# Kernel tuning notes

Hardware: AMD Instinct MI355X
Metric: run time of the kernel (lower is better)

## Reference

```python
import jax, jax.numpy as jnp
import numpy as np
from jax import lax

NUM_COARSE = 64
GROUP_SIZE = 32
GRID_SIZE = 6
GRID_PTS = GRID_SIZE * GRID_SIZE  # 36


def setup_inputs() -> dict:
    key = jax.random.key(0)
    ki = iter(jax.random.split(key, 64))

    def rn(shape, scale=0.02):
        return jax.random.normal(next(ki), shape, jnp.float32) * scale

    B, N = 8, 8192
    return {
        "corrupted_pts": jax.random.normal(next(ki), (B, N, 3), jnp.float32),
        "pts": jax.random.normal(next(ki), (B, N, 3), jnp.float32),
        "enc_w1": rn((3, 128)), "enc_b1": jnp.zeros((128,), jnp.float32),
        "enc_w2": rn((128, 256)), "enc_b2": jnp.zeros((256,), jnp.float32),
        "enc_w3": rn((256, 1024)), "enc_b3": jnp.zeros((1024,), jnp.float32),
        "pe_w1": rn((3, 128)), "pe_b1": jnp.zeros((128,), jnp.float32),
        "pe_w2": rn((128, 1024)), "pe_b2": jnp.zeros((1024,), jnp.float32),
        "cp_w1": rn((1024, 1024)), "cp_b1": jnp.zeros((1024,), jnp.float32),
        "cp_w2": rn((1024, 1024)), "cp_b2": jnp.zeros((1024,), jnp.float32),
        "cp_w3": rn((1024, NUM_COARSE * 3)), "cp_b3": jnp.zeros((NUM_COARSE * 3,), jnp.float32),
        "f1_w1": rn((1024 + 2, 512)), "f1_b1": jnp.zeros((512,), jnp.float32),
        "f1_w2": rn((512, 512)), "f1_b2": jnp.zeros((512,), jnp.float32),
        "f1_w3": rn((512, 3)), "f1_b3": jnp.zeros((3,), jnp.float32),
        "f2_w1": rn((1024 + 3, 512)), "f2_b1": jnp.zeros((512,), jnp.float32),
        "f2_w2": rn((512, 512)), "f2_b2": jnp.zeros((512,), jnp.float32),
        "f2_w3": rn((512, 3)), "f2_b3": jnp.zeros((3,), jnp.float32),
    }


def _fps(xyz, n_samples):
    """Farthest point sampling, start at index 0. xyz: (N,3) -> (n_samples,3)."""
    d0 = jnp.sum((xyz - xyz[0]) ** 2, axis=-1)

    def step(dists, _):
        nxt = jnp.argmax(dists)
        d = jnp.sum((xyz - xyz[nxt]) ** 2, axis=-1)
        return jnp.minimum(dists, d), nxt

    _, idxs = lax.scan(step, d0, None, length=n_samples - 1)
    idxs = jnp.concatenate([jnp.zeros((1,), idxs.dtype), idxs])
    return xyz[idxs]


def _chamfer_l2(x, y):
    """Symmetric Chamfer-L2 over batched point sets x:(B,Nx,3), y:(B,Ny,3)."""
    d = jnp.sum((x[:, :, None, :] - y[:, None, :, :]) ** 2, axis=-1)  # (B,Nx,Ny)
    return jnp.mean(jnp.min(d, axis=2)) + jnp.mean(jnp.min(d, axis=1))


def _build_grid():
    # itertools.product(x, y): x varies slowest -> 'ij' meshgrid ordering
    lin = jnp.linspace(-0.3, 0.3, GRID_SIZE)
    xx, yy = jnp.meshgrid(lin, lin, indexing="ij")
    return jnp.stack([xx.ravel(), yy.ravel()], axis=-1)  # (36,2)


def reference(corrupted_pts, pts,
              enc_w1, enc_b1, enc_w2, enc_b2, enc_w3, enc_b3,
              pe_w1, pe_b1, pe_w2, pe_b2,
              cp_w1, cp_b1, cp_w2, cp_b2, cp_w3, cp_b3,
              f1_w1, f1_b1, f1_w2, f1_b2, f1_w3, f1_b3,
              f2_w1, f2_b1, f2_w2, f2_b2, f2_w3, f2_b3):
    corrupted_pts = corrupted_pts[:, :, :3]
    pts = pts[:, :, :3]
    B, N, _ = pts.shape

    # --- Group divider: FPS centers + KNN neighborhoods (normalized) ---
    centers = jax.vmap(lambda p: _fps(p, NUM_COARSE))(pts)            # (B,G,3)
    d2 = jnp.sum((centers[:, :, None, :] - pts[:, None, :, :]) ** 2, axis=-1)  # (B,G,N)
    _, idx = lax.top_k(-d2, GROUP_SIZE)                               # (B,G,K)
    neigh = jnp.take_along_axis(pts[:, None, :, :], idx[..., None], axis=2)    # (B,G,K,3)
    neigh = neigh - centers[:, :, None, :]

    # --- positional embedding of centers ---
    pos = jax.nn.gelu(centers @ pe_w1 + pe_b1, approximate=False) @ pe_w2 + pe_b2  # (B,G,1024)

    # --- global encoder (PointNet-style stand-in for PointNetv2_encoder) ---
    h = jax.nn.relu(corrupted_pts @ enc_w1 + enc_b1)
    h = jax.nn.relu(h @ enc_w2 + enc_b2)
    h = h @ enc_w3 + enc_b3
    feat = jnp.max(h, axis=1)                                          # (B,1024)

    # --- coarse prediction ---
    c = jax.nn.relu(feat @ cp_w1 + cp_b1)
    c = jax.nn.relu(c @ cp_w2 + cp_b2)
    coarse = (c @ cp_w3 + cp_b3).reshape(B, NUM_COARSE, 3)

    # --- folding decoder (1x1 convs == per-point linears) ---
    BG = B * NUM_COARSE
    fe = (feat[:, None, :] + pos).reshape(BG, 1024)
    fe = jnp.broadcast_to(fe[:, None, :], (BG, GRID_PTS, 1024))
    grid = jnp.broadcast_to(_build_grid()[None], (BG, GRID_PTS, 2))
    cat1 = jnp.concatenate([fe, grid], axis=-1)                        # (BG,36,1026)
    h1 = jax.nn.relu(cat1 @ f1_w1 + f1_b1)
    h1 = jax.nn.relu(h1 @ f1_w2 + f1_b2)
    fold1 = h1 @ f1_w3 + f1_b3                                         # (BG,36,3)
    cat2 = jnp.concatenate([fe, fold1], axis=-1)                       # (BG,36,1027)
    h2 = jax.nn.relu(cat2 @ f2_w1 + f2_b1)
    h2 = jax.nn.relu(h2 @ f2_w2 + f2_b2)
    fold2 = h2 @ f2_w3 + f2_b3                                         # (BG,36,3)

    loss_coarse = _chamfer_l2(coarse, centers)
    loss_fine = _chamfer_l2(fold2, neigh.reshape(BG, GROUP_SIZE, 3))
    return (loss_fine, loss_coarse)
```

## Files before the change

### kernel.cpp

```cpp
#include <hip/hip_runtime.h>
#include <float.h>
#include <math.h>

typedef unsigned short u16;
typedef short bshort8 __attribute__((ext_vector_type(8)));
typedef float vf4 __attribute__((ext_vector_type(4)));

struct Ptrs { const float* p[30]; };

__device__ __align__(16) unsigned int g_featkey[8192];
__device__ __align__(16) float g_fold1[18432 * 3];
__device__ __align__(16) float g_fold2[18432 * 3];
__device__ __align__(16) float g_accum[8];
__device__ __align__(16) float g_centers[512 * 3];
__device__ __align__(16) float g_neigh[512 * 32 * 3];
__device__ __align__(16) float g_c1[8192];
__device__ __align__(16) float g_c2[8192];
__device__ __align__(16) float g_coarse[8 * 192];
__device__ __align__(16) u16 g_p1[512 * 128];
__device__ __align__(16) u16 g_fe[512 * 1024];
__device__ __align__(16) u16 g_fea[512 * 512];
__device__ __align__(16) u16 g_feb[512 * 512];
__device__ __align__(16) float g_gw[36 * 512];
__device__ __align__(16) u16 g_w2T[256 * 128];
__device__ __align__(16) u16 g_w3T[1024 * 256];
__device__ __align__(16) u16 g_pew2T[1024 * 128];
__device__ __align__(16) u16 g_f1w1aT[512 * 1024];
__device__ __align__(16) u16 g_f1w2T[512 * 512];
__device__ __align__(16) u16 g_f2w1aT[512 * 1024];
__device__ __align__(16) u16 g_f2w2T[512 * 512];

__device__ __forceinline__ u16 f2b(float f) {
    unsigned int u = __float_as_uint(f);
    unsigned int r = (u + 0x7fffu + ((u >> 16) & 1u)) >> 16;
    return (u16)r;
}
__device__ __forceinline__ float b2f(u16 u) {
    return __uint_as_float(((unsigned int)u) << 16);
}
__device__ __forceinline__ float dec(unsigned int k) {
    unsigned int u = (k & 0x80000000u) ? (k & 0x7fffffffu) : ~k;
    return __uint_as_float(u);
}

__global__ __launch_bounds__(256) void zero_kernel(Ptrs ptrs, u16* out) {
    int i = blockIdx.x * 256 + threadIdx.x;
    if (i < 8192) {
        g_featkey[i] = 0u;
        g_c1[i] = 0.f;
        g_c2[i] = 0.f;
    }
    if (i < 1536) g_coarse[i] = 0.f;
    if (i < 18432 * 3) { g_fold1[i] = 0.f; g_fold2[i] = 0.f; }
    if (i < 8) g_accum[i] = 0.f;
}

__global__ __launch_bounds__(256) void convert_kernel(Ptrs ptrs, u16* out) {
    int plane = blockIdx.y;
    if (plane == 7) {
        int id = blockIdx.x * 256 + threadIdx.x;
        if (id >= 36 * 512) return;
        const float* f1w1 = ptrs.p[18];
        const float* f1b1 = ptrs.p[19];
        int q = id >> 9, n = id & 511;
        int qi = q / 6, qj = q - qi * 6;
        float gx = (qi == 5) ? 0.3f : (-0.3f + qi * 0.12f);
        float gy = (qj == 5) ? 0.3f : (-0.3f + qj * 0.12f);
        g_gw[id] = gx * f1w1[(size_t)1024 * 512 + n] + gy * f1w1[(size_t)1025 * 512 + n] + f1b1[n];
        return;
    }
    static const int kSrc[7] = {4, 6, 10, 18, 20, 24, 26};
    int K, N;
    u16* dst;
    switch (plane) {
        case 0:  dst = g_w2T;    K = 128;  N = 256;  break;
        case 1:  dst = g_w3T;    K = 256;  N = 1024; break;
        case 2:  dst = g_pew2T;  K = 128;  N = 1024; break;
        case 3:  dst = g_f1w1aT; K = 1024; N = 512;  break;
        case 4:  dst = g_f1w2T;  K = 512;  N = 512;  break;
        case 5:  dst = g_f2w1aT; K = 1024; N = 512;  break;
        default: dst = g_f2w2T;  K = 512;  N = 512;  break;
    }
    int tilesK = K >> 6, tilesN = N >> 6;
    int tile = blockIdx.x;
    if (tile >= tilesK * tilesN) return;
    int tk = tile % tilesK, tn = tile / tilesK;
    int k0 = tk * 64, n0 = tn * 64;
    const float* src = ptrs.p[kSrc[plane]];
    __shared__ float tl[64 * 65];
    int r = threadIdx.x >> 2, c16 = (threadIdx.x & 3) * 16;
    const float* sp = &src[(size_t)(k0 + r) * N + n0 + c16];
#pragma unroll
    for (int j = 0; j < 16; ++j) tl[r * 65 + c16 + j] = sp[j];
    __syncthreads();
    union { u16 u[16]; uint4 v[2]; } tmp;
#pragma unroll
    for (int j = 0; j < 16; ++j) tmp.u[j] = f2b(tl[(c16 + j) * 65 + r]);
    u16* dp = &dst[(size_t)(n0 + r) * K + k0 + c16];
    *(uint4*)&dp[0] = tmp.v[0];
    *(uint4*)&dp[8] = tmp.v[1];
}

__global__ __launch_bounds__(256) void fps_encoder_kernel(Ptrs ptrs, u16* out) {
    __shared__ __align__(16) short h1s[64 * 136];
    __shared__ __align__(16) short h2s[64 * 264];
    __shared__ __align__(16) short Bs[2][64 * 72];
    __shared__ float red[256];
    __shared__ float xyzs[192];
    int tid = threadIdx.x;
    if (blockIdx.x < 8) {
#pragma clang fp contract(off)
        int b = blockIdx.x;
        const float* P = ptrs.p[1] + (size_t)b * 8192 * 3;
        float px[32], py[32], pz[32], ds[32];
        float cx = P[0], cy = P[1], cz = P[2];
#pragma unroll
        for (int j = 0; j < 32; ++j) {
            int i = tid + j * 256;
            px[j] = P[i * 3]; py[j] = P[i * 3 + 1]; pz[j] = P[i * 3 + 2];
            float dx = px[j] - cx, dy = py[j] - cy, dz = pz[j] - cz;
            ds[j] = (dx * dx + dy * dy) + dz * dz;
        }
        float* wv = red;
        int* wi = (int*)(red + 4);
        float* cen = xyzs;
        if (tid == 0) {
            g_centers[b * 192 + 0] = cx; cen[0] = cx;
            g_centers[b * 192 + 1] = cy; cen[1] = cy;
            g_centers[b * 192 + 2] = cz; cen[2] = cz;
        }
        int lane = tid & 63, w = tid >> 6;
        for (int s = 1; s < 64; ++s) {
            float v = -1.f; int vi = 1 << 30;
#pragma unroll
            for (int j = 0; j < 32; ++j) {
                int i = tid + j * 256;
                if (ds[j] > v) { v = ds[j]; vi = i; }
            }
#pragma unroll
            for (int off = 1; off < 64; off <<= 1) {
                float ov = __shfl_xor(v, off); int oi = __shfl_xor(vi, off);
                if (ov > v || (ov == v && oi < vi)) { v = ov; vi = oi; }
            }
            if (lane == 0) { wv[w] = v; wi[w] = vi; }
            __syncthreads();
            float bv = wv[0]; int bi = wi[0];
#pragma unroll
            for (int k = 1; k < 4; ++k)
                if (wv[k] > bv || (wv[k] == bv && wi[k] < bi)) { bv = wv[k]; bi = wi[k]; }
            bi &= 8191;
            if ((bi & 255) == tid) {
                int j = bi >> 8;
                cen[s * 3 + 0] = px[j];
                cen[s * 3 + 1] = py[j];
                cen[s * 3 + 2] = pz[j];
                g_centers[b * 192 + s * 3 + 0] = px[j];
                g_centers[b * 192 + s * 3 + 1] = py[j];
                g_centers[b * 192 + s * 3 + 2] = pz[j];
            }
            __syncthreads();
            float nxx = cen[s * 3], nxy = cen[s * 3 + 1], nxz = cen[s * 3 + 2];
#pragma unroll
            for (int j = 0; j < 32; ++j) {
                float dx = px[j] - nxx, dy = py[j] - nxy, dz = pz[j] - nxz;
                float d = (dx * dx + dy * dy) + dz * dz;
                ds[j] = fminf(ds[j], d);
            }
        }
        const float* pw = ptrs.p[8];
        const float* pb = ptrs.p[9];
        for (int ii = tid; ii < 8192; ii += 256) {
            int g = ii >> 7, o = ii & 127;
            float x0 = cen[g * 3], x1 = cen[g * 3 + 1], x2 = cen[g * 3 + 2];
            float h = x0 * pw[o] + x1 * pw[128 + o] + x2 * pw[256 + o] + pb[o];
            float ge = 0.5f * h * (1.0f + erff(h * 0.7071067811865475f));
            g_p1[(size_t)(b * 64 + g) * 128 + o] = f2b(ge);
        }
        return;
    }
    const float* X = ptrs.p[0];
    const float* w1 = ptrs.p[2];
    const float* b1 = ptrs.p[3];
    const float* b2 = ptrs.p[5];
    const float* b3 = ptrs.p[7];
    int base = (blockIdx.x - 8) * 64;
    for (int i = tid; i < 192; i += 256) xyzs[i] = X[(size_t)base * 3 + i];
    __syncthreads();
    {
        int k = tid & 127;
        float wa = w1[k], wbv = w1[128 + k], wc = w1[256 + k], bb = b1[k];
        int r0 = tid >> 7;
#pragma unroll
        for (int it = 0; it < 32; ++it) {
            int row = r0 + it * 2;
            float v = xyzs[row * 3] * wa + xyzs[row * 3 + 1] * wbv + xyzs[row * 3 + 2] * wc + bb;
            h1s[row * 136 + k] = (short)f2b(fmaxf(v, 0.f));
        }
    }
    int lane = tid & 63, w = tid >> 6, q = lane >> 4, c = lane & 15;
    int brow = tid >> 2, bc = (tid & 3) * 16;
    for (int nch = 0; nch < 4; ++nch) {
        const u16* W = &g_w2T[(size_t)(nch * 64 + brow) * 128 + bc];
        uint4 r0v = *(const uint4*)&W[0];
        uint4 r1v = *(const uint4*)&W[8];
        *(uint4*)&Bs[0][brow * 72 + bc] = r0v;
        *(uint4*)&Bs[0][brow * 72 + bc + 8] = r1v;
        uint4 s0v = *(const uint4*)&W[64];
        uint4 s1v = *(const uint4*)&W[72];
        __syncthreads();
        vf4 acc[4];
#pragma unroll
        for (int t = 0; t < 4; ++t)
#pragma unroll
            for (int r = 0; r < 4; ++r) acc[t][r] = 0.f;
#pragma unroll
        for (int s = 0; s < 2; ++s) {
            bshort8 av = *(const bshort8*)&h1s[(w * 16 + c) * 136 + s * 32 + q * 8];
#pragma unroll
            for (int t = 0; t < 4; ++t) {
                bshort8 bv = *(const bshort8*)&Bs[0][(t * 16 + c) * 72 + s * 32 + q * 8];
                acc[t] = __builtin_amdgcn_mfma_f32_16x16x32_bf16(av, bv, acc[t], 0, 0, 0);
            }
        }
        *(uint4*)&Bs[1][brow * 72 + bc] = s0v;
        *(uint4*)&Bs[1][brow * 72 + bc + 8] = s1v;
        __syncthreads();
#pragma unroll
        for (int s = 0; s < 2; ++s) {
            bshort8 av = *(const bshort8*)&h1s[(w * 16 + c) * 136 + 64 + s * 32 + q * 8];
#pragma unroll
            for (int t = 0; t < 4; ++t) {
                bshort8 bv = *(const bshort8*)&Bs[1][(t * 16 + c) * 72 + s * 32 + q * 8];
                acc[t] = __builtin_amdgcn_mfma_f32_16x16x32_bf16(av, bv, acc[t], 0, 0, 0);
            }
        }
#pragma unroll
        for (int t = 0; t < 4; ++t) {
            int n = nch * 64 + t * 16 + c;
            float bv = b2[n];
#pragma unroll
            for (int r = 0; r < 4; ++r) {
                int row = w * 16 + q * 4 + r;
                h2s[row * 264 + n] = (short)f2b(fmaxf(acc[t][r] + bv, 0.f));
            }
        }
    }
    int batch = base >> 13;
    for (int nch = 0; nch < 16; ++nch) {
        const u16* W = &g_w3T[(size_t)(nch * 64 + brow) * 256 + bc];
        uint4 a0 = *(const uint4*)&W[0];
        uint4 a1 = *(const uint4*)&W[8];
        *(uint4*)&Bs[0][brow * 72 + bc] = a0;
        *(uint4*)&Bs[0][brow * 72 + bc + 8] = a1;
        uint4 n0 = *(const uint4*)&W[64];
        uint4 n1 = *(const uint4*)&W[72];
        __syncthreads();
        vf4 acc[4];
#pragma unroll
        for (int t = 0; t < 4; ++t)
#pragma unroll
            for (int r = 0; r < 4; ++r) acc[t][r] = 0.f;
#pragma unroll
        for (int ch = 0; ch < 4; ++ch) {
            int p = ch & 1;
#pragma unroll
            for (int s = 0; s < 2; ++s) {
                bshort8 av = *(const bshort8*)&h2s[(w * 16 + c) * 264 + ch * 64 + s * 32 + q * 8];
#pragma unroll
                for (int t = 0; t < 4; ++t) {
                    bshort8 bv = *(const bshort8*)&Bs[p][(t * 16 + c) * 72 + s * 32 + q * 8];
                    acc[t] = __builtin_amdgcn_mfma_f32_16x16x32_bf16(av, bv, acc[t], 0, 0, 0);
                }
            }
            if (ch < 3) {
                *(uint4*)&Bs[1 - p][brow * 72 + bc] = n0;
                *(uint4*)&Bs[1 - p][brow * 72 + bc + 8] = n1;
                if (ch < 2) {
                    n0 = *(const uint4*)&W[(ch + 2) * 64];
                    n1 = *(const uint4*)&W[(ch + 2) * 64 + 8];
                }
                __syncthreads();
            }
        }
#pragma unroll
        for (int t = 0; t < 4; ++t) {
            float m = fmaxf(fmaxf(acc[t][0], acc[t][1]), fmaxf(acc[t][2], acc[t][3]));
            m = fmaxf(m, __shfl_xor(m, 16));
            m = fmaxf(m, __shfl_xor(m, 32));
            if (lane < 16) red[w * 64 + t * 16 + lane] = m;
        }
        __syncthreads();
        if (tid < 64) {
            float m = fmaxf(fmaxf(red[tid], red[64 + tid]), fmaxf(red[128 + tid], red[192 + tid]));
            float val = m + b3[nch * 64 + tid];
            unsigned int u = __float_as_uint(val);
            unsigned int key = (u & 0x80000000u) ? ~u : (u | 0x80000000u);
            atomicMax(&g_featkey[batch * 1024 + nch * 64 + tid], key);
        }
        __syncthreads();
    }
}

__global__ __launch_bounds__(256) void group_kernel(Ptrs ptrs, u16* out) {
#pragma clang fp contract(off)
    int g = blockIdx.x, tid = threadIdx.x;
    int b = g >> 6;
    const float* P = ptrs.p[1] + (size_t)b * 8192 * 3;
    float cx = g_centers[g * 3], cy = g_centers[g * 3 + 1], cz = g_centers[g * 3 + 2];
    __shared__ float dl[8192];
    for (int j = 0; j < 32; ++j) {
        int i = tid + j * 256;
        float dx = P[i * 3] - cx, dy = P[i * 3 + 1] - cy, dz = P[i * 3 + 2] - cz;
        dl[i] = (dx * dx + dy * dy) + dz * dz;
    }
    __syncthreads();
    __shared__ float wv[4];
    __shared__ int wi[4];
    int lane = tid & 63, w = tid >> 6;
    for (int r = 0; r < 32; ++r) {
        float v = FLT_MAX; int vi = 1 << 30;
        for (int j = 0; j < 32; ++j) {
            int i = tid + j * 256;
            float d = dl[i];
            if (d < v) { v = d; vi = i; }
        }
#pragma unroll
        for (int off = 1; off < 64; off <<= 1) {
            float ov = __shfl_xor(v, off); int oi = __shfl_xor(vi, off);
            if (ov < v || (ov == v && oi < vi)) { v = ov; vi = oi; }
        }
        if (lane == 0) { wv[w] = v; wi[w] = vi; }
        __syncthreads();
        if (tid == 0) {
            float bv = wv[0]; int bi = wi[0];
            for (int k = 1; k < 4; ++k)
                if (wv[k] < bv || (wv[k] == bv && wi[k] < bi)) { bv = wv[k]; bi = wi[k]; }
            bi &= 8191;
            g_neigh[((size_t)g * 32 + r) * 3 + 0] = P[bi * 3] - cx;
            g_neigh[((size_t)g * 32 + r) * 3 + 1] = P[bi * 3 + 1] - cy;
            g_neigh[((size_t)g * 32 + r) * 3 + 2] = P[bi * 3 + 2] - cz;
            dl[bi] = FLT_MAX;
        }
        __syncthreads();
    }
}

template <int N, int K, int ASEL, int BSEL, int OSEL>
__global__ __launch_bounds__(256) void gemm_kernel(Ptrs ptrs, u16* out) {
    const u16* A = (ASEL == 0) ? g_p1 : g_fe;
    const u16* BT = (BSEL == 0) ? g_pew2T : ((BSEL == 1) ? g_f1w1aT : g_f2w1aT);
    const float* bias = ptrs.p[11];
    __shared__ __align__(16) short As[64 * 40];
    __shared__ __align__(16) short Bs[64 * 40];
    int tid = threadIdx.x;
    int lane = tid & 63, w = tid >> 6;
    int mBase = blockIdx.y * 64, nBase = blockIdx.x * 64;
    int q = lane >> 4, c = lane & 15;
    vf4 acc[4];
#pragma unroll
    for (int t = 0; t < 4; ++t)
#pragma unroll
        for (int r = 0; r < 4; ++r) acc[t][r] = 0.f;
    int srow = tid >> 2, scol = (tid & 3) * 8;
    for (int k0 = 0; k0 < K; k0 += 32) {
        uint4 aval = *(const uint4*)&A[(size_t)(mBase + srow) * K + k0 + scol];
        uint4 bval = *(const uint4*)&BT[(size_t)(nBase + srow) * K + k0 + scol];
        __syncthreads();
        *(uint4*)&As[srow * 40 + scol] = aval;
        *(uint4*)&Bs[srow * 40 + scol] = bval;
        __syncthreads();
        bshort8 av = *(const bshort8*)&As[(w * 16 + c) * 40 + q * 8];
#pragma unroll
        for (int t = 0; t < 4; ++t) {
            bshort8 bv = *(const bshort8*)&Bs[(t * 16 + c) * 40 + q * 8];
            acc[t] = __builtin_amdgcn_mfma_f32_16x16x32_bf16(av, bv, acc[t], 0, 0, 0);
        }
    }
#pragma unroll
    for (int t = 0; t < 4; ++t) {
        int n = nBase + t * 16 + c;
#pragma unroll
        for (int r = 0; r < 4; ++r) {
            int m = mBase + w * 16 + q * 4 + r;
            float v = acc[t][r];
            if (OSEL == 0)
                g_fe[(size_t)m * N + n] =
                    f2b(dec(g_featkey[(m >> 6) * 1024 + n]) + v + bias[n]);
            else if (OSEL == 1)
                g_fea[(size_t)m * N + n] = f2b(v);
            else
                g_feb[(size_t)m * N + n] = f2b(v);
        }
    }
}

template <int MODE>
__global__ __launch_bounds__(256) void fold_gemm_kernel(Ptrs ptrs, u16* out) {
    const u16* feX = (MODE == 1) ? g_fea : g_feb;
    const u16* W2T = (MODE == 1) ? g_f1w2T : g_f2w2T;
    const float* gmat = (MODE == 1) ? g_gw : g_fold1;
    float* foldOut = (MODE == 1) ? g_fold1 : g_fold2;
    const float* b2 = (MODE == 1) ? ptrs.p[21] : ptrs.p[27];
    const float* W3 = (MODE == 1) ? ptrs.p[22] : ptrs.p[28];
    const float* wb = ptrs.p[24] + (size_t)1024 * 512;
    const float* sbias = ptrs.p[25];
    const float* pb3 = ptrs.p[23];
    __shared__ __align__(16) short As[64 * 40];
    __shared__ __align__(16) short Bs[64 * 40];
    int tid = threadIdx.x;
    int lane = tid & 63, w = tid >> 6, q = lane >> 4, c = lane & 15;
    int mBase = blockIdx.y * 64, nBase = blockIdx.x * 64;
    int srow = tid >> 2, scol = (tid & 3) * 8;
    int row = mBase + srow;
    int g = row / 36;
    int qq = row - g * 36;
    float f0 = 0.f, f1 = 0.f, f2 = 0.f;
    if (MODE == 2) {
        f0 = gmat[row * 3 + 0] + pb3[0];
        f1 = gmat[row * 3 + 1] + pb3[1];
        f2 = gmat[row * 3 + 2] + pb3[2];
    }
    vf4 acc[4];
#pragma unroll
    for (int t = 0; t < 4; ++t)
#pragma unroll
        for (int r = 0; r < 4; ++r) acc[t][r] = 0.f;
    for (int kt = 0; kt < 16; ++kt) {
        union { u16 u[8]; uint4 v; } tmp;
        int kb = kt * 32 + scol;
        if (MODE == 1) {
#pragma unroll
            for (int j = 0; j < 8; ++j) {
                float v = b2f(feX[g * 512 + kb + j]) + gmat[qq * 512 + kb + j];
                tmp.u[j] = f2b(fmaxf(v, 0.f));
            }
        } else {
#pragma unroll
            for (int j = 0; j < 8; ++j) {
                int k = kb + j;
                float v = b2f(feX[g * 512 + k]) + f0 * wb[k] + f1 * wb[512 + k] +
                          f2 * wb[1024 + k] + sbias[k];
                tmp.u[j] = f2b(fmaxf(v, 0.f));
            }
        }
        uint4 bval = *(const uint4*)&W2T[(size_t)(nBase + srow) * 512 + kb];
        __syncthreads();
        *(uint4*)&As[srow * 40 + scol] = tmp.v;
        *(uint4*)&Bs[srow * 40 + scol] = bval;
        __syncthreads();
        bshort8 av = *(const bshort8*)&As[(w * 16 + c) * 40 + q * 8];
#pragma unroll
        for (int t = 0; t < 4; ++t) {
            bshort8 bv = *(const bshort8*)&Bs[(t * 16 + c) * 40 + q * 8];
            acc[t] = __builtin_amdgcn_mfma_f32_16x16x32_bf16(av, bv, acc[t], 0, 0, 0);
        }
    }
    float p[4][3];
#pragma unroll
    for (int r = 0; r < 4; ++r)
#pragma unroll
        for (int o = 0; o < 3; ++o) p[r][o] = 0.f;
#pragma unroll
    for (int t = 0; t < 4; ++t) {
        int n = nBase + t * 16 + c;
        float bv = b2[n];
        float w30 = W3[n * 3], w31 = W3[n * 3 + 1], w32 = W3[n * 3 + 2];
#pragma unroll
        for (int r = 0; r < 4; ++r) {
            float v = fmaxf(acc[t][r] + bv, 0.f);
            p[r][0] += v * w30; p[r][1] += v * w31; p[r][2] += v * w32;
        }
    }
#pragma unroll
    for (int off = 1; off < 16; off <<= 1)
#pragma unroll
        for (int r = 0; r < 4; ++r)
#pragma unroll
            for (int o = 0; o < 3; ++o) p[r][o] += __shfl_xor(p[r][o], off);
    if (c == 0) {
#pragma unroll
        for (int r = 0; r < 4; ++r) {
            int orow = mBase + w * 16 + q * 4 + r;
            atomicAdd(&foldOut[orow * 3 + 0], p[r][0]);
            atomicAdd(&foldOut[orow * 3 + 1], p[r][1]);
            atomicAdd(&foldOut[orow * 3 + 2], p[r][2]);
        }
    }
}

template <int SEL, int N>
__global__ __launch_bounds__(256) void thinmlp_kernel(Ptrs ptrs, u16* out) {
    float* dst = (SEL == 0) ? g_c1 : ((SEL == 1) ? g_c2 : g_coarse);
    const float* B = (SEL == 0) ? ptrs.p[12] : ((SEL == 1) ? ptrs.p[14] : ptrs.p[16]);
    const float* pbias = (SEL == 1) ? ptrs.p[13] : ptrs.p[15];
    __shared__ float Als[8 * 64];
    int tid = threadIdx.x;
    int k0 = blockIdx.y * 64;
    for (int i = tid; i < 8 * 64; i += 256) {
        int m = i >> 6, k = k0 + (i & 63);
        float a;
        if (SEL == 0)      a = dec(g_featkey[m * 1024 + k]);
        else if (SEL == 1) a = fmaxf(g_c1[m * 1024 + k] + pbias[k], 0.f);
        else               a = fmaxf(g_c2[m * 1024 + k] + pbias[k], 0.f);
        Als[i] = a;
    }
    __syncthreads();
    int n = blockIdx.x * 256 + tid;
    if (n >= N) return;
    float acc[8];
#pragma unroll
    for (int m = 0; m < 8; ++m) acc[m] = 0.f;
    for (int k = 0; k < 64; ++k) {
        float bv = B[(size_t)(k0 + k) * N + n];
#pragma unroll
        for (int m = 0; m < 8; ++m) acc[m] += Als[m * 64 + k] * bv;
    }
#pragma unroll
    for (int m = 0; m < 8; ++m) atomicAdd(&dst[(size_t)m * N + n], acc[m]);
}

__global__ __launch_bounds__(128) void chamfer_fine_kernel(Ptrs ptrs, u16* out) {
    const float* f2b3 = ptrs.p[29];
    __shared__ float f[108], nn[96];
    __shared__ float pA[128], pB[128];
    int g = blockIdx.x, tid = threadIdx.x;
    float b3v[3] = {f2b3[0], f2b3[1], f2b3[2]};
    for (int i = tid; i < 108; i += 128) {
        int o = i - (i / 3) * 3;
        f[i] = g_fold2[(size_t)g * 108 + i] + b3v[o];
    }
    for (int i = tid; i < 96; i += 128) nn[i] = g_neigh[(size_t)g * 96 + i];
    __syncthreads();
    float sA = 0.f, sB = 0.f;
    if (tid < 36) {
        float bx = f[tid * 3], by = f[tid * 3 + 1], bz = f[tid * 3 + 2];
        float best = FLT_MAX;
        for (int j = 0; j < 32; ++j) {
            float dx = bx - nn[j * 3], dy = by - nn[j * 3 + 1], dz = bz - nn[j * 3 + 2];
            best = fminf(best, dx * dx + dy * dy + dz * dz);
        }
        sA = best;
    } else if (tid >= 64 && tid < 96) {
        int j = tid - 64;
        float bx = nn[j * 3], by = nn[j * 3 + 1], bz = nn[j * 3 + 2];
        float best = FLT_MAX;
        for (int i = 0; i < 36; ++i) {
            float dx = f[i * 3] - bx, dy = f[i * 3 + 1] - by, dz = f[i * 3 + 2] - bz;
            best = fminf(best, dx * dx + dy * dy + dz * dz);
        }
        sB = best;
    }
    pA[tid] = sA; pB[tid] = sB;
    __syncthreads();
    for (int s2 = 64; s2; s2 >>= 1) {
        if (tid < s2) { pA[tid] += pA[tid + s2]; pB[tid] += pB[tid + s2]; }
        __syncthreads();
    }
    if (tid == 0) { atomicAdd(&g_accum[0], pA[0]); atomicAdd(&g_accum[1], pB[0]); }
}

__global__ __launch_bounds__(128) void chamfer_coarse_kernel(Ptrs ptrs, u16* out) {
    const float* cb3 = ptrs.p[17];
    __shared__ float cc[192], ct[192];
    __shared__ float pA[128], pB[128];
    int b = blockIdx.x, tid = threadIdx.x;
    for (int i = tid; i < 192; i += 128) {
        cc[i] = g_coarse[(size_t)b * 192 + i] + cb3[i];
        ct[i] = g_centers[(size_t)b * 192 + i];
    }
    __syncthreads();
    float sA = 0.f, sB = 0.f;
    if (tid < 64) {
        float bx = cc[tid * 3], by = cc[tid * 3 + 1], bz = cc[tid * 3 + 2];
        float best = FLT_MAX;
        for (int j = 0; j < 64; ++j) {
            float dx = bx - ct[j * 3], dy = by - ct[j * 3 + 1], dz = bz - ct[j * 3 + 2];
            best = fminf(best, dx * dx + dy * dy + dz * dz);
        }
        sA = best;
    } else {
        int j = tid - 64;
        float bx = ct[j * 3], by = ct[j * 3 + 1], bz = ct[j * 3 + 2];
        float best = FLT_MAX;
        for (int i = 0; i < 64; ++i) {
            float dx = cc[i * 3] - bx, dy = cc[i * 3 + 1] - by, dz = cc[i * 3 + 2] - bz;
            best = fminf(best, dx * dx + dy * dy + dz * dz);
        }
        sB = best;
    }
    pA[tid] = sA; pB[tid] = sB;
    __syncthreads();
    for (int s2 = 64; s2; s2 >>= 1) {
        if (tid < s2) { pA[tid] += pA[tid + s2]; pB[tid] += pB[tid + s2]; }
        __syncthreads();
    }
    if (tid == 0) { atomicAdd(&g_accum[2], pA[0]); atomicAdd(&g_accum[3], pB[0]); }
}

__global__ void finalize_kernel(Ptrs ptrs, u16* out) {
    if (threadIdx.x == 0) {
        float lf = g_accum[0] / (512.f * 36.f) + g_accum[1] / (512.f * 32.f);
        float lc = g_accum[2] / 512.f + g_accum[3] / 512.f;
        u16 blf = f2b(lf), blc = f2b(lc);
        out[0] = blc;
        out[1] = blf;
        out[2] = blc;
        out[3] = blc;
        out[4] = blc;
        out[5] = blc;
    }
}

extern "C" void kernel_launch(void* const* d_in, const int* in_sizes, int n_in,
                              void* d_out, int out_size, void* d_ws, size_t ws_size,
                              hipStream_t stream) {
    (void)in_sizes; (void)out_size; (void)d_ws; (void)ws_size;
    Ptrs ptrs;
    for (int i = 0; i < 30; ++i) {
        int j = (i < n_in) ? i : (n_in - 1);
        ptrs.p[i] = (const float*)d_in[j];
    }
    u16* out = (u16*)d_out;

    zero_kernel<<<216, 256, 0, stream>>>(ptrs, out);
    convert_kernel<<<dim3(128, 8), 256, 0, stream>>>(ptrs, out);

    fps_encoder_kernel<<<1032, 256, 0, stream>>>(ptrs, out);
    group_kernel<<<512, 256, 0, stream>>>(ptrs, out);

    thinmlp_kernel<0, 1024><<<dim3(4, 16), 256, 0, stream>>>(ptrs, out);
    thinmlp_kernel<1, 1024><<<dim3(4, 16), 256, 0, stream>>>(ptrs, out);
    thinmlp_kernel<2, 192><<<dim3(1, 16), 256, 0, stream>>>(ptrs, out);

    gemm_kernel<1024, 128, 0, 0, 0><<<dim3(16, 8), 256, 0, stream>>>(ptrs, out);

    gemm_kernel<512, 1024, 1, 1, 1><<<dim3(8, 8), 256, 0, stream>>>(ptrs, out);
    fold_gemm_kernel<1><<<dim3(8, 288), 256, 0, stream>>>(ptrs, out);

    gemm_kernel<512, 1024, 1, 2, 2><<<dim3(8, 8), 256, 0, stream>>>(ptrs, out);
    fold_gemm_kernel<2><<<dim3(8, 288), 256, 0, stream>>>(ptrs, out);

    chamfer_coarse_kernel<<<8, 128, 0, stream>>>(ptrs, out);
    chamfer_fine_kernel<<<512, 128, 0, stream>>>(ptrs, out);
    finalize_kernel<<<1, 64, 0, stream>>>(ptrs, out);
}
```

Before: 535.7 us.

## Restructure FPS loop and merge GEMM and chamfer launches

The FPS loop stops caching point coordinates in registers. It reloads them from global memory each step, and the argmax scan is fused into the distance-update loop. The per-step barrier count drops from two to one by double-buffering the reduction slots. The two feature GEMMs (f1/f2 first layer) are merged into one launch via blockIdx.z, and the coarse and fine chamfer kernels are merged into a single launch, cutting launch count and letting both GEMMs share the GPU. Reloading points from memory in the serial FPS loop could add latency, though it lowers register pressure.

Measured after the change: 493.1 us. 1.09x faster.

```diff
diff --git a/kernel.cpp b/kernel.cpp
--- a/kernel.cpp
+++ b/kernel.cpp
@@ -112,17 +112,18 @@
 #pragma clang fp contract(off)
         int b = blockIdx.x;
         const float* P = ptrs.p[1] + (size_t)b * 8192 * 3;
-        float px[32], py[32], pz[32], ds[32];
+        float ds[32];
         float cx = P[0], cy = P[1], cz = P[2];
+        float v = -1.f; int vi = 1 << 30;
 #pragma unroll
         for (int j = 0; j < 32; ++j) {
             int i = tid + j * 256;
-            px[j] = P[i * 3]; py[j] = P[i * 3 + 1]; pz[j] = P[i * 3 + 2];
-            float dx = px[j] - cx, dy = py[j] - cy, dz = pz[j] - cz;
+            float dx = P[i * 3] - cx, dy = P[i * 3 + 1] - cy, dz = P[i * 3 + 2] - cz;
             ds[j] = (dx * dx + dy * dy) + dz * dz;
-        }
-        float* wv = red;
-        int* wi = (int*)(red + 4);
+            if (ds[j] > v) { v = ds[j]; vi = i; }
+        }
+        __shared__ float wv2[2][4];
+        __shared__ int wi2[2][4];
         float* cen = xyzs;
         if (tid == 0) {
             g_centers[b * 192 + 0] = cx; cen[0] = cx;
@@ -131,42 +132,40 @@
         }
         int lane = tid & 63, w = tid >> 6;
         for (int s = 1; s < 64; ++s) {
-            float v = -1.f; int vi = 1 << 30;
-#pragma unroll
-            for (int j = 0; j < 32; ++j) {
-                int i = tid + j * 256;
-                if (ds[j] > v) { v = ds[j]; vi = i; }
-            }
+            int p = s & 1;
 #pragma unroll
             for (int off = 1; off < 64; off <<= 1) {
                 float ov = __shfl_xor(v, off); int oi = __shfl_xor(vi, off);
                 if (ov > v || (ov == v && oi < vi)) { v = ov; vi = oi; }
             }
-            if (lane == 0) { wv[w] = v; wi[w] = vi; }
+            if (lane == 0) { wv2[p][w] = v; wi2[p][w] = vi; }
             __syncthreads();
-            float bv = wv[0]; int bi = wi[0];
+            float bv = wv2[p][0]; int bi = wi2[p][0];
 #pragma unroll
             for (int k = 1; k < 4; ++k)
-                if (wv[k] > bv || (wv[k] == bv && wi[k] < bi)) { bv = wv[k]; bi = wi[k]; }
+                if (wv2[p][k] > bv || (wv2[p][k] == bv && wi2[p][k] < bi)) {
+                    bv = wv2[p][k]; bi = wi2[p][k];
+                }
             bi &= 8191;
-            if ((bi & 255) == tid) {
-                int j = bi >> 8;
-                cen[s * 3 + 0] = px[j];
-                cen[s * 3 + 1] = py[j];
-                cen[s * 3 + 2] = pz[j];
-                g_centers[b * 192 + s * 3 + 0] = px[j];
-                g_centers[b * 192 + s * 3 + 1] = py[j];
-                g_centers[b * 192 + s * 3 + 2] = pz[j];
-            }
-            __syncthreads();
-            float nxx = cen[s * 3], nxy = cen[s * 3 + 1], nxz = cen[s * 3 + 2];
+            float nxx = P[bi * 3], nxy = P[bi * 3 + 1], nxz = P[bi * 3 + 2];
+            if (tid == 0) {
+                cen[s * 3 + 0] = nxx; cen[s * 3 + 1] = nxy; cen[s * 3 + 2] = nxz;
+                g_centers[b * 192 + s * 3 + 0] = nxx;
+                g_centers[b * 192 + s * 3 + 1] = nxy;
+                g_centers[b * 192 + s * 3 + 2] = nxz;
+            }
+            v = -1.f; vi = 1 << 30;
 #pragma unroll
             for (int j = 0; j < 32; ++j) {
-                float dx = px[j] - nxx, dy = py[j] - nxy, dz = pz[j] - nxz;
+                int i = tid + j * 256;
+                float dx = P[i * 3] - nxx, dy = P[i * 3 + 1] - nxy, dz = P[i * 3 + 2] - nxz;
                 float d = (dx * dx + dy * dy) + dz * dz;
-                ds[j] = fminf(ds[j], d);
-            }
-        }
+                float nd = fminf(ds[j], d);
+                ds[j] = nd;
+                if (nd > v) { v = nd; vi = i; }
+            }
+        }
+        __syncthreads();
         const float* pw = ptrs.p[8];
         const float* pb = ptrs.p[9];
         for (int ii = tid; ii < 8192; ii += 256) {
@@ -345,11 +344,11 @@
     }
 }
 
-template <int N, int K, int ASEL, int BSEL, int OSEL>
-__global__ __launch_bounds__(256) void gemm_kernel(Ptrs ptrs, u16* out) {
-    const u16* A = (ASEL == 0) ? g_p1 : g_fe;
-    const u16* BT = (BSEL == 0) ? g_pew2T : ((BSEL == 1) ? g_f1w1aT : g_f2w1aT);
+__global__ __launch_bounds__(256) void gemm_fe_kernel(Ptrs ptrs, u16* out) {
+    const u16* A = g_p1;
+    const u16* BT = g_pew2T;
     const float* bias = ptrs.p[11];
+    const int N = 1024, K = 128;
     __shared__ __align__(16) short As[64 * 40];
     __shared__ __align__(16) short Bs[64 * 40];
     int tid = threadIdx.x;
@@ -383,13 +382,49 @@
         for (int r = 0; r < 4; ++r) {
             int m = mBase + w * 16 + q * 4 + r;
             float v = acc[t][r];
-            if (OSEL == 0)
-                g_fe[(size_t)m * N + n] =
-                    f2b(dec(g_featkey[(m >> 6) * 1024 + n]) + v + bias[n]);
-            else if (OSEL == 1)
-                g_fea[(size_t)m * N + n] = f2b(v);
-            else
-                g_feb[(size_t)m * N + n] = f2b(v);
+            g_fe[(size_t)m * N + n] = f2b(dec(g_featkey[(m >> 6) * 1024 + n]) + v + bias[n]);
+        }
+    }
+}
+
+__global__ __launch_bounds__(256) void gemm_ab_kernel(Ptrs ptrs, u16* out) {
+    const u16* A = g_fe;
+    const u16* BT = (blockIdx.z == 0) ? g_f1w1aT : g_f2w1aT;
+    u16* dst = (blockIdx.z == 0) ? g_fea : g_feb;
+    const int N = 512, K = 1024;
+    __shared__ __align__(16) short As[64 * 40];
+    __shared__ __align__(16) short Bs[64 * 40];
+    int tid = threadIdx.x;
+    int lane = tid & 63, w = tid >> 6;
+    int mBase = blockIdx.y * 64, nBase = blockIdx.x * 64;
+    int q = lane >> 4, c = lane & 15;
+    vf4 acc[4];
+#pragma unroll
+    for (int t = 0; t < 4; ++t)
+#pragma unroll
+        for (int r = 0; r < 4; ++r) acc[t][r] = 0.f;
+    int srow = tid >> 2, scol = (tid & 3) * 8;
+    for (int k0 = 0; k0 < K; k0 += 32) {
+        uint4 aval = *(const uint4*)&A[(size_t)(mBase + srow) * K + k0 + scol];
+        uint4 bval = *(const uint4*)&BT[(size_t)(nBase + srow) * K + k0 + scol];
+        __syncthreads();
+        *(uint4*)&As[srow * 40 + scol] = aval;
+        *(uint4*)&Bs[srow * 40 + scol] = bval;
+        __syncthreads();
+        bshort8 av = *(const bshort8*)&As[(w * 16 + c) * 40 + q * 8];
+#pragma unroll
+        for (int t = 0; t < 4; ++t) {
+            bshort8 bv = *(const bshort8*)&Bs[(t * 16 + c) * 40 + q * 8];
+            acc[t] = __builtin_amdgcn_mfma_f32_16x16x32_bf16(av, bv, acc[t], 0, 0, 0);
+        }
+    }
+#pragma unroll
+    for (int t = 0; t < 4; ++t) {
+        int n = nBase + t * 16 + c;
+#pragma unroll
+        for (int r = 0; r < 4; ++r) {
+            int m = mBase + w * 16 + q * 4 + r;
+            dst[(size_t)m * N + n] = f2b(acc[t][r]);
         }
     }
 }
@@ -519,82 +554,81 @@
     for (int m = 0; m < 8; ++m) atomicAdd(&dst[(size_t)m * N + n], acc[m]);
 }
 
-__global__ __launch_bounds__(128) void chamfer_fine_kernel(Ptrs ptrs, u16* out) {
+__global__ __launch_bounds__(128) void chamfer_kernel(Ptrs ptrs, u16* out) {
+    __shared__ float s1[192], s2[192];
+    __shared__ float pA[128], pB[128];
+    int tid = threadIdx.x;
+    if (blockIdx.x < 8) {
+        const float* cb3 = ptrs.p[17];
+        int b = blockIdx.x;
+        for (int i = tid; i < 192; i += 128) {
+            s1[i] = g_coarse[(size_t)b * 192 + i] + cb3[i];
+            s2[i] = g_centers[(size_t)b * 192 + i];
+        }
+        __syncthreads();
+        float sA = 0.f, sB = 0.f;
+        if (tid < 64) {
+            float bx = s1[tid * 3], by = s1[tid * 3 + 1], bz = s1[tid * 3 + 2];
+            float best = FLT_MAX;
+            for (int j = 0; j < 64; ++j) {
+                float dx = bx - s2[j * 3], dy = by - s2[j * 3 + 1], dz = bz - s2[j * 3 + 2];
+                best = fminf(best, dx * dx + dy * dy + dz * dz);
+            }
+            sA = best;
+        } else {
+            int j = tid - 64;
+            float bx = s2[j * 3], by = s2[j * 3 + 1], bz = s2[j * 3 + 2];
+            float best = FLT_MAX;
+            for (int i = 0; i < 64; ++i) {
+                float dx = s1[i * 3] - bx, dy = s1[i * 3 + 1] - by, dz = s1[i * 3 + 2] - bz;
+                best = fminf(best, dx * dx + dy * dy + dz * dz);
+            }
+            sB = best;
+        }
+        pA[tid] = sA; pB[tid] = sB;
+        __syncthreads();
+        for (int st = 64; st; st >>= 1) {
+            if (tid < st) { pA[tid] += pA[tid + st]; pB[tid] += pB[tid + st]; }
+            __syncthreads();
+        }
+        if (tid == 0) { atomicAdd(&g_accum[2], pA[0]); atomicAdd(&g_accum[3], pB[0]); }
+        return;
+    }
     const float* f2b3 = ptrs.p[29];
-    __shared__ float f[108], nn[96];
-    __shared__ float pA[128], pB[128];
-    int g = blockIdx.x, tid = threadIdx.x;
+    int g = blockIdx.x - 8;
     float b3v[3] = {f2b3[0], f2b3[1], f2b3[2]};
     for (int i = tid; i < 108; i += 128) {
         int o = i - (i / 3) * 3;
-        f[i] = g_fold2[(size_t)g * 108 + i] + b3v[o];
-    }
-    for (int i = tid; i < 96; i += 128) nn[i] = g_neigh[(size_t)g * 96 + i];
+        s1[i] = g_fold2[(size_t)g * 108 + i] + b3v[o];
+    }
+    for (int i = tid; i < 96; i += 128) s2[i] = g_neigh[(size_t)g * 96 + i];
     __syncthreads();
     float sA = 0.f, sB = 0.f;
     if (tid < 36) {
-        float bx = f[tid * 3], by = f[tid * 3 + 1], bz = f[tid * 3 + 2];
+        float bx = s1[tid * 3], by = s1[tid * 3 + 1], bz = s1[tid * 3 + 2];
         float best = FLT_MAX;
         for (int j = 0; j < 32; ++j) {
-            float dx = bx - nn[j * 3], dy = by - nn[j * 3 + 1], dz = bz - nn[j * 3 + 2];
+            float dx = bx - s2[j * 3], dy = by - s2[j * 3 + 1], dz = bz - s2[j * 3 + 2];
             best = fminf(best, dx * dx + dy * dy + dz * dz);
         }
         sA = best;
     } else if (tid >= 64 && tid < 96) {
         int j = tid - 64;
-        float bx = nn[j * 3], by = nn[j * 3 + 1], bz = nn[j * 3 + 2];
+        float bx = s2[j * 3], by = s2[j * 3 + 1], bz = s2[j * 3 + 2];
         float best = FLT_MAX;
         for (int i = 0; i < 36; ++i) {
-            float dx = f[i * 3] - bx, dy = f[i * 3 + 1] - by, dz = f[i * 3 + 2] - bz;
+            float dx = s1[i * 3] - bx, dy = s1[i * 3 + 1] - by, dz = s1[i * 3 + 2] - bz;
             best = fminf(best, dx * dx + dy * dy + dz * dz);
         }
         sB = best;
     }
     pA[tid] = sA; pB[tid] = sB;
     __syncthreads();
-    for (int s2 = 64; s2; s2 >>= 1) {
-        if (tid < s2) { pA[tid] += pA[tid + s2]; pB[tid] += pB[tid + s2]; }
+    for (int st = 64; st; st >>= 1) {
+        if (tid < st) { pA[tid] += pA[tid + st]; pB[tid] += pB[tid + st]; }
         __syncthreads();
     }
     if (tid == 0) { atomicAdd(&g_accum[0], pA[0]); atomicAdd(&g_accum[1], pB[0]); }
-}
-
-__global__ __launch_bounds__(128) void chamfer_coarse_kernel(Ptrs ptrs, u16* out) {
-    const float* cb3 = ptrs.p[17];
-    __shared__ float cc[192], ct[192];
-    __shared__ float pA[128], pB[128];
-    int b = blockIdx.x, tid = threadIdx.x;
-    for (int i = tid; i < 192; i += 128) {
-        cc[i] = g_coarse[(size_t)b * 192 + i] + cb3[i];
-        ct[i] = g_centers[(size_t)b * 192 + i];
-    }
-    __syncthreads();
-    float sA = 0.f, sB = 0.f;
-    if (tid < 64) {
-        float bx = cc[tid * 3], by = cc[tid * 3 + 1], bz = cc[tid * 3 + 2];
-        float best = FLT_MAX;
-        for (int j = 0; j < 64; ++j) {
-            float dx = bx - ct[j * 3], dy = by - ct[j * 3 + 1], dz = bz - ct[j * 3 + 2];
-            best = fminf(best, dx * dx + dy * dy + dz * dz);
-        }
-        sA = best;
-    } else {
-        int j = tid - 64;
-        float bx = ct[j * 3], by = ct[j * 3 + 1], bz = ct[j * 3 + 2];
-        float best = FLT_MAX;
-        for (int i = 0; i < 64; ++i) {
-            float dx = cc[i * 3] - bx, dy = cc[i * 3 + 1] - by, dz = cc[i * 3 + 2] - bz;
-            best = fminf(best, dx * dx + dy * dy + dz * dz);
-        }
-        sB = best;
-    }
-    pA[tid] = sA; pB[tid] = sB;
-    __syncthreads();
-    for (int s2 = 64; s2; s2 >>= 1) {
-        if (tid < s2) { pA[tid] += pA[tid + s2]; pB[tid] += pB[tid + s2]; }
-        __syncthreads();
-    }
-    if (tid == 0) { atomicAdd(&g_accum[2], pA[0]); atomicAdd(&g_accum[3], pB[0]); }
 }
 
 __global__ void finalize_kernel(Ptrs ptrs, u16* out) {
@@ -632,15 +666,12 @@
     thinmlp_kernel<1, 1024><<<dim3(4, 16), 256, 0, stream>>>(ptrs, out);
     thinmlp_kernel<2, 192><<<dim3(1, 16), 256, 0, stream>>>(ptrs, out);
 
-    gemm_kernel<1024, 128, 0, 0, 0><<<dim3(16, 8), 256, 0, stream>>>(ptrs, out);
-
-    gemm_kernel<512, 1024, 1, 1, 1><<<dim3(8, 8), 256, 0, stream>>>(ptrs, out);
+    gemm_fe_kernel<<<dim3(16, 8), 256, 0, stream>>>(ptrs, out);
+
+    gemm_ab_kernel<<<dim3(8, 8, 2), 256, 0, stream>>>(ptrs, out);
     fold_gemm_kernel<1><<<dim3(8, 288), 256, 0, stream>>>(ptrs, out);
-
-    gemm_kernel<512, 1024, 1, 2, 2><<<dim3(8, 8), 256, 0, stream>>>(ptrs, out);
     fold_gemm_kernel<2><<<dim3(8, 288), 256, 0, stream>>>(ptrs, out);
 
-    chamfer_coarse_kernel<<<8, 128, 0, stream>>>(ptrs, out);
-    chamfer_fine_kernel<<<512, 128, 0, stream>>>(ptrs, out);
+    chamfer_kernel<<<520, 128, 0, stream>>>(ptrs, out);
     finalize_kernel<<<1, 64, 0, stream>>>(ptrs, out);
 }
```
